# Performance work log

Hardware: AMD Instinct MI355X
Metric: run time of the kernel (lower is better)

The kernel has to match this reference:

```python
import jax, jax.numpy as jnp
import numpy as np
from jax import lax

DN = ('NCHW', 'OIHW', 'NCHW')

def conv3x3(x, w):
    return lax.conv_general_dilated(x, w, (1, 1), 'SAME', dimension_numbers=DN)

def conv1x1(x, w, b):
    # w: [O, C], x: [B, C, H, W]
    return jnp.einsum('oc,bchw->bohw', w, x) + b[None, :, None, None]

def bn_relu(x, p):
    # p: [2, C] -> (scale, shift), eval-mode folded BatchNorm + ReLU
    return jax.nn.relu(x * p[0][None, :, None, None] + p[1][None, :, None, None])

def pam(y, Wb, bb, Wc, bc, Wd, bd, alpha):
    B, C, H, W = y.shape
    n = H * W
    b_ = conv1x1(y, Wb, bb).reshape(B, -1, n)   # [B, C/8, N]
    c_ = conv1x1(y, Wc, bc).reshape(B, -1, n)   # [B, C/8, N]
    d_ = conv1x1(y, Wd, bd).reshape(B, C, n)    # [B, C, N]
    energy = jnp.einsum('bkn,bkm->bnm', b_, c_)  # [B, N, N]
    attn = jax.nn.softmax(energy, axis=-1)
    feat = jnp.einsum('bcm,bnm->bcn', d_, attn).reshape(B, C, H, W)
    return alpha[0] * feat + y

def cam(y, beta):
    B, C, H, W = y.shape
    xf = y.reshape(B, C, H * W)
    energy = jnp.einsum('bcn,bdn->bcd', xf, xf)  # [B, C, C]
    energy = jnp.max(energy, axis=-1, keepdims=True) - energy
    attn = jax.nn.softmax(energy, axis=-1)
    feat = jnp.einsum('bcd,bdn->bcn', attn, xf).reshape(B, C, H, W)
    return beta[0] * feat + y

def reference(x, Wp1, bnp1, Wc1, bnc1, Wb, bb, Wc, bc, Wd, bd, alpha, beta,
              Wp2, bnp2, Wc2, bnc2, Wout, bout, Wp3, bp3, Wc3, bc3):
    feat_p = bn_relu(conv3x3(x, Wp1), bnp1)
    feat_p = pam(feat_p, Wb, bb, Wc, bc, Wd, bd, alpha)
    feat_p = bn_relu(conv3x3(feat_p, Wp2), bnp2)

    feat_c = bn_relu(conv3x3(x, Wc1), bnc1)
    feat_c = cam(feat_c, beta)
    feat_c = bn_relu(conv3x3(feat_c, Wc2), bnc2)

    fusion = feat_p + feat_c
    out_main = jax.nn.sigmoid(conv1x1(fusion, Wout, bout))
    out_p = jax.nn.sigmoid(conv1x1(feat_p, Wp3, bp3))
    out_c = jax.nn.sigmoid(conv1x1(feat_c, Wc3, bc3))
    return (out_main, out_p, out_c)

def setup_inputs() -> dict:
    key = jax.random.key(0)
    ks = jax.random.split(key, 24)
    Cin, Ci, Ck, NC = 512, 128, 16, 19
    B, H, W = 8, 64, 64
    s = lambda k, shape, scale=0.05: jax.random.normal(k, shape, jnp.float32) * scale
    return {
        'x': jax.random.normal(ks[0], (B, Cin, H, W), jnp.float32),
        'Wp1': s(ks[1], (Ci, Cin, 3, 3)), 'bnp1': jnp.stack([jnp.ones(Ci), jnp.zeros(Ci)]),
        'Wc1': s(ks[2], (Ci, Cin, 3, 3)), 'bnc1': jnp.stack([jnp.ones(Ci), jnp.zeros(Ci)]),
        'Wb': s(ks[3], (Ck, Ci)), 'bb': s(ks[4], (Ck,)),
        'Wc': s(ks[5], (Ck, Ci)), 'bc': s(ks[6], (Ck,)),
        'Wd': s(ks[7], (Ci, Ci)), 'bd': s(ks[8], (Ci,)),
        'alpha': jax.random.normal(ks[9], (1,), jnp.float32) * 0.5,
        'beta': jax.random.normal(ks[10], (1,), jnp.float32) * 0.5,
        'Wp2': s(ks[11], (Ci, Ci, 3, 3)), 'bnp2': jnp.stack([jnp.ones(Ci), jnp.zeros(Ci)]),
        'Wc2': s(ks[12], (Ci, Ci, 3, 3)), 'bnc2': jnp.stack([jnp.ones(Ci), jnp.zeros(Ci)]),
        'Wout': s(ks[13], (NC, Ci)), 'bout': s(ks[14], (NC,)),
        'Wp3': s(ks[15], (NC, Ci)), 'bp3': s(ks[16], (NC,)),
        'Wc3': s(ks[17], (NC, Ci)), 'bc3': s(ks[18], (NC,)),
    }
```

## Files before the change

kernel.cpp:

```cpp
#include <hip/hip_runtime.h>
#include <math.h>


typedef __attribute__((ext_vector_type(8)))  short short8;
typedef __attribute__((ext_vector_type(16))) float f32x16;

__device__ inline unsigned short f2bf(float f) {
    union { float f; unsigned u; } v; v.f = f;
    unsigned r = v.u + 0x7fffu + ((v.u >> 16) & 1u);
    return (unsigned short)(r >> 16);
}
__device__ inline float bf2f(unsigned short h) {
    union { unsigned u; float f; } v; v.u = ((unsigned)h) << 16;
    return v.f;
}

__global__ __launch_bounds__(256) void wpack_kernel(
    const float* __restrict__ W, unsigned short* __restrict__ wp, int Cin, int total)
{
    int idx = blockIdx.x * 256 + threadIdx.x;
    if (idx >= total) return;
    int chunk = idx / 18432;
    int rem   = idx - chunk * 18432;
    int tap   = rem >> 11;
    int rem2  = rem & 2047;
    int co    = rem2 >> 4;
    int ci    = rem2 & 15;
    int cin   = (chunk << 4) + ci;
    wp[idx] = f2bf(W[((size_t)co * Cin + cin) * 9 + tap]);
}

__global__ __launch_bounds__(256) void wpack_split_kernel(
    const float* __restrict__ W, unsigned short* __restrict__ wph,
    unsigned short* __restrict__ wpl, int Cin, int total)
{
    int idx = blockIdx.x * 256 + threadIdx.x;
    if (idx >= total) return;
    int chunk = idx / 18432;
    int rem   = idx - chunk * 18432;
    int tap   = rem >> 11;
    int rem2  = rem & 2047;
    int co    = rem2 >> 4;
    int ci    = rem2 & 15;
    int cin   = (chunk << 4) + ci;
    float w = W[((size_t)co * Cin + cin) * 9 + tap];
    unsigned short hi = f2bf(w);
    wph[idx] = hi;
    wpl[idx] = f2bf(w - bf2f(hi));
}

__global__ __launch_bounds__(256) void conv3x3_mfma(
    const void* __restrict__ xin, int in_is_fp32, int Cin,
    const unsigned short* __restrict__ wpack, const float* __restrict__ bn,
    float* __restrict__ out_f32, unsigned short* __restrict__ out_bf)
{
    const int t   = threadIdx.x;
    const int w   = t >> 6;
    const int wy  = w >> 1;
    const int wx  = w & 1;
    const int ln  = t & 63;
    const int l31 = ln & 31;
    const int g   = ln >> 5;
    const int y0  = blockIdx.x << 1;
    const int co0 = blockIdx.y << 6;
    const int b   = blockIdx.z;

    __shared__ __align__(16) unsigned short Xl[4 * 66 * 16];
    __shared__ __align__(16) unsigned short Wl[9 * 64 * 16];

    const f32x16 zero = {0,0,0,0,0,0,0,0,0,0,0,0,0,0,0,0};
    f32x16 acc0 = zero, acc1 = zero;

    const int nchunks = Cin >> 4;
    for (int ch = 0; ch < nchunks; ++ch) {
        const int cin0 = ch << 4;
        for (int pid = t; pid < 264; pid += 256) {
            int r  = pid / 66;
            int xc = pid - r * 66;
            int gy = y0 - 1 + r;
            int gx = xc - 1;
            unsigned short tmp[16];
            if ((unsigned)gy < 64u && (unsigned)gx < 64u) {
                if (in_is_fp32) {
                    const float* src = (const float*)xin
                        + (((size_t)b * Cin + cin0) << 12) + (gy << 6) + gx;
#pragma unroll
                    for (int c = 0; c < 16; c++) tmp[c] = f2bf(src[(size_t)c << 12]);
                } else {
                    const unsigned short* src = (const unsigned short*)xin
                        + (((size_t)b * Cin + cin0) << 12) + (gy << 6) + gx;
#pragma unroll
                    for (int c = 0; c < 16; c++) tmp[c] = src[(size_t)c << 12];
                }
            } else {
#pragma unroll
                for (int c = 0; c < 16; c++) tmp[c] = 0;
            }
            *(uint4*)&Xl[pid * 16 + 0] = ((uint4*)tmp)[0];
            *(uint4*)&Xl[pid * 16 + 8] = ((uint4*)tmp)[1];
        }
        {
            const uint4* wsrc = (const uint4*)wpack;
            const int base = ch * 2304 + (co0 << 1);
            for (int idx = t; idx < 1152; idx += 256)
                ((uint4*)Wl)[idx] = wsrc[base + ((idx >> 7) << 8) + (idx & 127)];
        }
        __syncthreads();

#pragma unroll 3
        for (int tap = 0; tap < 9; ++tap) {
            const int dy = tap / 3, dx = tap - dy * 3;
            short8 a = *(const short8*)&Wl[((tap << 6) + (wy << 5) + l31) * 16 + (g << 3)];
            const int row = wx + dy;
            short8 b0 = *(const short8*)&Xl[(row * 66 + l31 + dx) * 16 + (g << 3)];
            short8 b1 = *(const short8*)&Xl[(row * 66 + l31 + 32 + dx) * 16 + (g << 3)];
            acc0 = __builtin_amdgcn_mfma_f32_32x32x16_bf16(a, b0, acc0, 0, 0, 0);
            acc1 = __builtin_amdgcn_mfma_f32_32x32x16_bf16(a, b1, acc1, 0, 0, 0);
        }
        __syncthreads();
    }

    const int y = y0 + wx;
#pragma unroll
    for (int j = 0; j < 2; j++) {
        const f32x16 a = j ? acc1 : acc0;
#pragma unroll
        for (int r = 0; r < 16; r++) {
            int co = co0 + (wy << 5) + (r & 3) + ((r >> 2) << 3) + (g << 2);
            int x  = (j << 5) + l31;
            float v = fmaf(a[r], bn[co], bn[128 + co]);
            v = v > 0.f ? v : 0.f;
            size_t o = (((size_t)b * 128 + co) << 12) + (y << 6) + x;
            if (out_f32) out_f32[o] = v;
            if (out_bf)  out_bf[o]  = f2bf(v);
        }
    }
}

__global__ __launch_bounds__(256) void conv3x3_mfma_hilo(
    const float* __restrict__ xin, int Cin,
    const unsigned short* __restrict__ wph, const unsigned short* __restrict__ wpl,
    const float* __restrict__ bn, float* __restrict__ out_f32,
    unsigned short* __restrict__ outh, unsigned short* __restrict__ outl)
{
    const int t   = threadIdx.x;
    const int w   = t >> 6;
    const int wy  = w >> 1;
    const int wx  = w & 1;
    const int ln  = t & 63;
    const int l31 = ln & 31;
    const int g   = ln >> 5;
    const int y0  = blockIdx.x << 1;
    const int co0 = blockIdx.y << 6;
    const int b   = blockIdx.z;

    __shared__ __align__(16) unsigned short Xh[4 * 66 * 16];
    __shared__ __align__(16) unsigned short Xo[4 * 66 * 16];
    __shared__ __align__(16) unsigned short Wh[9 * 64 * 16];
    __shared__ __align__(16) unsigned short Wo[9 * 64 * 16];

    const f32x16 zero = {0,0,0,0,0,0,0,0,0,0,0,0,0,0,0,0};
    f32x16 acc0 = zero, acc1 = zero;

    const int nchunks = Cin >> 4;
    for (int ch = 0; ch < nchunks; ++ch) {
        const int cin0 = ch << 4;
        for (int pid = t; pid < 264; pid += 256) {
            int r  = pid / 66;
            int xc = pid - r * 66;
            int gy = y0 - 1 + r;
            int gx = xc - 1;
            unsigned short th[16], tl[16];
            if ((unsigned)gy < 64u && (unsigned)gx < 64u) {
                const float* src = xin + (((size_t)b * Cin + cin0) << 12) + (gy << 6) + gx;
#pragma unroll
                for (int c = 0; c < 16; c++) {
                    float f = src[(size_t)c << 12];
                    unsigned short hi = f2bf(f);
                    th[c] = hi;
                    tl[c] = f2bf(f - bf2f(hi));
                }
            } else {
#pragma unroll
                for (int c = 0; c < 16; c++) { th[c] = 0; tl[c] = 0; }
            }
            *(uint4*)&Xh[pid * 16 + 0] = ((uint4*)th)[0];
            *(uint4*)&Xh[pid * 16 + 8] = ((uint4*)th)[1];
            *(uint4*)&Xo[pid * 16 + 0] = ((uint4*)tl)[0];
            *(uint4*)&Xo[pid * 16 + 8] = ((uint4*)tl)[1];
        }
        {
            const uint4* sh = (const uint4*)wph;
            const uint4* sl = (const uint4*)wpl;
            const int base = ch * 2304 + (co0 << 1);
            for (int idx = t; idx < 1152; idx += 256) {
                int o = base + ((idx >> 7) << 8) + (idx & 127);
                ((uint4*)Wh)[idx] = sh[o];
                ((uint4*)Wo)[idx] = sl[o];
            }
        }
        __syncthreads();

#pragma unroll 1
        for (int tap = 0; tap < 9; ++tap) {
            const int dy = tap / 3, dx = tap - dy * 3;
            const int wi = ((tap << 6) + (wy << 5) + l31) * 16 + (g << 3);
            const int row = wx + dy;
            const int xi0 = (row * 66 + l31 + dx) * 16 + (g << 3);
            const int xi1 = (row * 66 + l31 + 32 + dx) * 16 + (g << 3);
            short8 ah = *(const short8*)&Wh[wi];
            short8 al = *(const short8*)&Wo[wi];
            short8 b0h = *(const short8*)&Xh[xi0];
            short8 b1h = *(const short8*)&Xh[xi1];
            short8 b0l = *(const short8*)&Xo[xi0];
            short8 b1l = *(const short8*)&Xo[xi1];
            acc0 = __builtin_amdgcn_mfma_f32_32x32x16_bf16(ah, b0h, acc0, 0, 0, 0);
            acc1 = __builtin_amdgcn_mfma_f32_32x32x16_bf16(ah, b1h, acc1, 0, 0, 0);
            acc0 = __builtin_amdgcn_mfma_f32_32x32x16_bf16(ah, b0l, acc0, 0, 0, 0);
            acc1 = __builtin_amdgcn_mfma_f32_32x32x16_bf16(ah, b1l, acc1, 0, 0, 0);
            acc0 = __builtin_amdgcn_mfma_f32_32x32x16_bf16(al, b0h, acc0, 0, 0, 0);
            acc1 = __builtin_amdgcn_mfma_f32_32x32x16_bf16(al, b1h, acc1, 0, 0, 0);
        }
        __syncthreads();
    }

    const int y = y0 + wx;
#pragma unroll
    for (int j = 0; j < 2; j++) {
        const f32x16 a = j ? acc1 : acc0;
#pragma unroll
        for (int r = 0; r < 16; r++) {
            int co = co0 + (wy << 5) + (r & 3) + ((r >> 2) << 3) + (g << 2);
            int x  = (j << 5) + l31;
            float v = fmaf(a[r], bn[co], bn[128 + co]);
            v = v > 0.f ? v : 0.f;
            size_t o = (((size_t)b * 128 + co) << 12) + (y << 6) + x;
            out_f32[o] = v;
            if (outh) {
                unsigned short hi = f2bf(v);
                outh[o] = hi;
                outl[o] = f2bf(v - bf2f(hi));
            }
        }
    }
}

__global__ __launch_bounds__(256) void cam_energy_mfma(
    const unsigned short* __restrict__ bh, const unsigned short* __restrict__ bl,
    float* __restrict__ egy_part)
{
    const int t   = threadIdx.x;
    const int w   = t >> 6;
    const int ln  = t & 63;
    const int l31 = ln & 31;
    const int g   = ln >> 5;
    const int i0  = (blockIdx.x >> 2) << 5;
    const int j0  = (blockIdx.x & 3) << 5;
    const int nseg = blockIdx.y;
    const int b   = blockIdx.z;

    __shared__ float red[4][64][17];

    const f32x16 zero = {0,0,0,0,0,0,0,0,0,0,0,0,0,0,0,0};
    f32x16 acc = zero;
    const int nb = (nseg << 9) + (w << 7) + (g << 3);
    const size_t ri = ((size_t)b * 128 + i0 + l31) << 12;
    const size_t rj = ((size_t)b * 128 + j0 + l31) << 12;

#pragma unroll
    for (int c = 0; c < 8; c++) {
        const int n0 = nb + (c << 4);
        short8 ah  = *(const short8*)(bh + ri + n0);
        short8 al  = *(const short8*)(bl + ri + n0);
        short8 bhf = *(const short8*)(bh + rj + n0);
        short8 blf = *(const short8*)(bl + rj + n0);
        acc = __builtin_amdgcn_mfma_f32_32x32x16_bf16(ah, bhf, acc, 0, 0, 0);
        acc = __builtin_amdgcn_mfma_f32_32x32x16_bf16(ah, blf, acc, 0, 0, 0);
        acc = __builtin_amdgcn_mfma_f32_32x32x16_bf16(al, bhf, acc, 0, 0, 0);
    }
#pragma unroll
    for (int r = 0; r < 16; r++) red[w][ln][r] = acc[r];
    __syncthreads();

    const int lane = t & 63;
    const int rq   = t >> 6;
    float* base = egy_part + (((size_t)(nseg * 8 + b)) << 14);
#pragma unroll
    for (int e = 0; e < 4; e++) {
        const int reg = (rq << 2) + e;
        float v = red[0][lane][reg] + red[1][lane][reg]
                + red[2][lane][reg] + red[3][lane][reg];
        const int i = i0 + (reg & 3) + ((reg >> 2) << 3) + ((lane >> 5) << 2);
        base[i * 128 + j0 + (lane & 31)] = v;
    }
}

__global__ __launch_bounds__(256) void cam_softmax_fused(
    const float* __restrict__ egy_part, float* __restrict__ egy)
{
    const int b   = blockIdx.x;
    const int rg  = blockIdx.y;
    const int t   = threadIdx.x;
    const int row = (rg << 4) + (t >> 4);
    const int jg  = t & 15;

    float e[8];
#pragma unroll
    for (int jj = 0; jj < 8; jj++) e[jj] = 0.f;
    for (int seg = 0; seg < 8; seg++) {
        const float* p = egy_part + (((size_t)(seg * 8 + b)) << 14) + row * 128 + (jg << 3);
#pragma unroll
        for (int jj = 0; jj < 8; jj++) e[jj] += p[jj];
    }
    float mn = e[0];
#pragma unroll
    for (int jj = 1; jj < 8; jj++) mn = fminf(mn, e[jj]);
#pragma unroll
    for (int k = 1; k < 16; k <<= 1) mn = fminf(mn, __shfl_xor(mn, k));
    float s = 0.f;
#pragma unroll
    for (int jj = 0; jj < 8; jj++) { float p = __expf(mn - e[jj]); e[jj] = p; s += p; }
#pragma unroll
    for (int k = 1; k < 16; k <<= 1) s += __shfl_xor(s, k);
    const float inv = 1.f / s;
    float* orow = egy + ((size_t)b << 14) + row * 128 + (jg << 3);
#pragma unroll
    for (int jj = 0; jj < 8; jj++) orow[jj] = e[jj] * inv;
}

__global__ __launch_bounds__(256) void pam_qk_1x1(
    const float* __restrict__ A, const float* __restrict__ Wb, const float* __restrict__ bb,
    const float* __restrict__ Wc, const float* __restrict__ bc,
    unsigned short* __restrict__ qt, unsigned short* __restrict__ kt)
{
    __shared__ float wl[2 * 16 * 128];
    __shared__ float bl[32];
    const int t = threadIdx.x;
    const int n = (blockIdx.x << 8) + t;
    const int b = blockIdx.y;
    for (int idx = t; idx < 2048; idx += 256) { wl[idx] = Wb[idx]; wl[2048 + idx] = Wc[idx]; }
    if (t < 16) { bl[t] = bb[t]; bl[16 + t] = bc[t]; }
    __syncthreads();
    float ab[16], ac[16];
#pragma unroll
    for (int k = 0; k < 16; k++) { ab[k] = 0.f; ac[k] = 0.f; }
    for (int chn = 0; chn < 128; ++chn) {
        float a = A[(((size_t)b * 128 + chn) << 12) + n];
#pragma unroll
        for (int k = 0; k < 16; k++) {
            ab[k] = fmaf(wl[k * 128 + chn], a, ab[k]);
            ac[k] = fmaf(wl[2048 + k * 128 + chn], a, ac[k]);
        }
    }
    unsigned short uq[16], uk[16];
#pragma unroll
    for (int k = 0; k < 16; k++) {
        uq[k] = f2bf(ab[k] + bl[k]);
        uk[k] = f2bf(ac[k] + bl[16 + k]);
    }
    size_t row = (size_t)b * 4096 + n;
    ((uint4*)qt)[row * 2 + 0] = ((uint4*)uq)[0];
    ((uint4*)qt)[row * 2 + 1] = ((uint4*)uq)[1];
    ((uint4*)kt)[row * 2 + 0] = ((uint4*)uk)[0];
    ((uint4*)kt)[row * 2 + 1] = ((uint4*)uk)[1];
}

__global__ __launch_bounds__(256) void pam_v_1x1(
    const float* __restrict__ A, const float* __restrict__ Wd, const float* __restrict__ bd,
    unsigned short* __restrict__ vb)
{
    __shared__ float wl[32 * 128];
    __shared__ float bl[32];
    const int t   = threadIdx.x;
    const int n   = (blockIdx.x << 8) + t;
    const int co0 = blockIdx.y << 5;
    const int b   = blockIdx.z;
    for (int idx = t; idx < 4096; idx += 256) {
        int c2 = idx >> 7, chv = idx & 127;
        wl[idx] = Wd[(co0 + c2) * 128 + chv];
    }
    if (t < 32) bl[t] = bd[co0 + t];
    __syncthreads();
    float acc[32];
#pragma unroll
    for (int k = 0; k < 32; k++) acc[k] = 0.f;
    for (int chn = 0; chn < 128; ++chn) {
        float a = A[(((size_t)b * 128 + chn) << 12) + n];
#pragma unroll
        for (int k = 0; k < 32; k++) acc[k] = fmaf(wl[k * 128 + chn], a, acc[k]);
    }
#pragma unroll
    for (int k = 0; k < 32; k++)
        vb[(((size_t)b * 128 + co0 + k) << 12) + n] = f2bf(acc[k] + bl[k]);
}

__global__ __launch_bounds__(256) void pam_rowmax(
    const unsigned short* __restrict__ qt, const unsigned short* __restrict__ kt,
    float* __restrict__ rowmax)
{
    const int t  = threadIdx.x;
    const int w  = t >> 6;
    const int L  = t & 63;
    const int ln = L & 31;
    const int g  = L >> 5;
    const int b  = blockIdx.y;
    const int n0 = blockIdx.x << 5;
    __shared__ float red[4][32];

    const f32x16 zero = {0,0,0,0,0,0,0,0,0,0,0,0,0,0,0,0};
    short8 qfrag = *(const short8*)(qt + (((size_t)b * 4096 + n0 + ln) << 4) + (g << 3));

    float mx = -INFINITY;
    for (int mq = (w << 5); mq < 4096; mq += 128) {
        short8 kfrag = *(const short8*)(kt + (((size_t)b * 4096 + mq + ln) << 4) + (g << 3));
        f32x16 s = __builtin_amdgcn_mfma_f32_32x32x16_bf16(kfrag, qfrag, zero, 0, 0, 0);
#pragma unroll
        for (int r = 0; r < 16; r++) mx = fmaxf(mx, s[r]);
    }
    mx = fmaxf(mx, __shfl_xor(mx, 32));
    if (L < 32) red[w][L] = mx;
    __syncthreads();
    if (t < 32) {
        float m = fmaxf(fmaxf(red[0][t], red[1][t]), fmaxf(red[2][t], red[3][t]));
        rowmax[((size_t)b << 12) + n0 + t] = m;
    }
}

__global__ __launch_bounds__(256) void pam_attn_mfma(
    const unsigned short* __restrict__ qt, const unsigned short* __restrict__ kt,
    const unsigned short* __restrict__ vb, const float* __restrict__ rowmax,
    const float* __restrict__ alpha, const float* __restrict__ Y,
    unsigned short* __restrict__ outb)
{
    const int t  = threadIdx.x;
    const int w  = t >> 6;
    const int L  = t & 63;
    const int ln = L & 31;
    const int g  = L >> 5;
    const int b  = blockIdx.y;
    const int n0 = blockIdx.x << 5;
    const int c0 = w << 5;

    __shared__ unsigned short Pf[16 * 256];
    __shared__ float red[4][32];

    const f32x16 zero = {0,0,0,0,0,0,0,0,0,0,0,0,0,0,0,0};
    short8 qfrag = *(const short8*)(qt + (((size_t)b * 4096 + n0 + ln) << 4) + (g << 3));
    const float rm = rowmax[((size_t)b << 12) + n0 + ln];
    const float al = alpha[0];

    f32x16 acc = zero;
    float rs = 0.f;

    for (int m0 = 0; m0 < 4096; m0 += 128) {
        const int mq = m0 + (w << 5);
        short8 kfrag = *(const short8*)(kt + (((size_t)b * 4096 + mq + ln) << 4) + (g << 3));
        f32x16 s = __builtin_amdgcn_mfma_f32_32x32x16_bf16(kfrag, qfrag, zero, 0, 0, 0);

        float p[16];
#pragma unroll
        for (int r = 0; r < 16; r++) { p[r] = __expf(s[r] - rm); rs += p[r]; }
        float xx[16];
#pragma unroll
        for (int r = 0; r < 16; r++) xx[r] = __shfl_xor(p[r], 32);

        unsigned short f0[8], f1[8];
#pragma unroll
        for (int i = 0; i < 4; i++) {
            f0[i]     = f2bf(g ? xx[4 + i]  : p[i]);
            f0[4 + i] = f2bf(g ? p[4 + i]   : xx[i]);
            f1[i]     = f2bf(g ? xx[12 + i] : p[8 + i]);
            f1[4 + i] = f2bf(g ? p[12 + i]  : xx[8 + i]);
        }
        *(short8*)(&Pf[((w << 2) + g) * 256 + (ln << 3)])     = *(short8*)f0;
        *(short8*)(&Pf[((w << 2) + 2 + g) * 256 + (ln << 3)]) = *(short8*)f1;
        __syncthreads();

#pragma unroll
        for (int kk = 0; kk < 8; kk++) {
            short8 pfrag = *(const short8*)(&Pf[((kk << 1) + g) * 256 + (ln << 3)]);
            short8 vfrag = *(const short8*)(vb + (((size_t)b * 128 + c0 + ln) << 12)
                                               + m0 + (kk << 4) + (g << 3));
            acc = __builtin_amdgcn_mfma_f32_32x32x16_bf16(vfrag, pfrag, acc, 0, 0, 0);
        }
        __syncthreads();
    }

    rs += __shfl_xor(rs, 32);
    if (L < 32) red[w][L] = rs;
    __syncthreads();
    const float inv = 1.f / (red[0][ln] + red[1][ln] + red[2][ln] + red[3][ln]);
    const int n = n0 + ln;
#pragma unroll
    for (int r = 0; r < 16; r++) {
        int c = c0 + (r & 3) + ((r >> 2) << 3) + (g << 2);
        size_t idx = (((size_t)b * 128 + c) << 12) + n;
        outb[idx] = f2bf(fmaf(al, acc[r] * inv, Y[idx]));
    }
}

__global__ __launch_bounds__(256) void cam_feat(
    const float* __restrict__ attn, const float* __restrict__ Bf,
    const float* __restrict__ beta, float* __restrict__ outf)
{
    const int t  = threadIdx.x;
    const int n  = (blockIdx.x << 8) + t;
    const int c0 = blockIdx.y << 5;
    const int b  = blockIdx.z;
    __shared__ float al[32 * 128];
    for (int idx = t; idx < 4096; idx += 256)
        al[idx] = attn[(size_t)b * 16384 + (c0 + (idx >> 7)) * 128 + (idx & 127)];
    __syncthreads();
    float acc[32];
#pragma unroll
    for (int k = 0; k < 32; k++) acc[k] = 0.f;
    for (int d = 0; d < 128; ++d) {
        float v = Bf[(((size_t)b * 128 + d) << 12) + n];
#pragma unroll
        for (int k = 0; k < 32; k++) acc[k] = fmaf(al[k * 128 + d], v, acc[k]);
    }
    float be = beta[0];
#pragma unroll
    for (int k = 0; k < 32; k++) {
        size_t idx = (((size_t)b * 128 + c0 + k) << 12) + n;
        outf[idx] = fmaf(be, acc[k], Bf[idx]);
    }
}

__global__ __launch_bounds__(256) void heads(
    const float* __restrict__ FP, const float* __restrict__ FC,
    const float* __restrict__ Wout, const float* __restrict__ bout,
    const float* __restrict__ Wp3, const float* __restrict__ bp3,
    const float* __restrict__ Wc3, const float* __restrict__ bc3,
    float* __restrict__ out)
{
    const int t = threadIdx.x;
    const int n = (blockIdx.x << 8) + t;
    const int b = blockIdx.y;
    __shared__ float wl[3 * 19 * 128];
    __shared__ float bl[3 * 19];
    for (int idx = t; idx < 2432; idx += 256) {
        wl[idx]        = Wout[idx];
        wl[2432 + idx] = Wp3[idx];
        wl[4864 + idx] = Wc3[idx];
    }
    if (t < 19) { bl[t] = bout[t]; bl[19 + t] = bp3[t]; bl[38 + t] = bc3[t]; }
    __syncthreads();
    float am[19], ap[19], ac[19];
#pragma unroll
    for (int o = 0; o < 19; o++) { am[o] = 0.f; ap[o] = 0.f; ac[o] = 0.f; }
    for (int chn = 0; chn < 128; ++chn) {
        float pv = FP[(((size_t)b * 128 + chn) << 12) + n];
        float cv = FC[(((size_t)b * 128 + chn) << 12) + n];
        float fv = pv + cv;
#pragma unroll
        for (int o = 0; o < 19; o++) {
            am[o] = fmaf(wl[o * 128 + chn], fv, am[o]);
            ap[o] = fmaf(wl[2432 + o * 128 + chn], pv, ap[o]);
            ac[o] = fmaf(wl[4864 + o * 128 + chn], cv, ac[o]);
        }
    }
    const size_t OS = (size_t)8 * 19 * 4096;
#pragma unroll
    for (int o = 0; o < 19; o++) {
        size_t base = (((size_t)b * 19 + o) << 12) + n;
        out[base]          = 1.f / (1.f + __expf(-(am[o] + bl[o])));
        out[OS + base]     = 1.f / (1.f + __expf(-(ap[o] + bl[19 + o])));
        out[2 * OS + base] = 1.f / (1.f + __expf(-(ac[o] + bl[38 + o])));
    }
}

extern "C" void kernel_launch(void* const* d_in, const int* in_sizes, int n_in,
                              void* d_out, int out_size, void* d_ws, size_t ws_size,
                              hipStream_t stream)
{
    const float* x     = (const float*)d_in[0];
    const float* Wp1   = (const float*)d_in[1];
    const float* bnp1  = (const float*)d_in[2];
    const float* Wc1   = (const float*)d_in[3];
    const float* bnc1  = (const float*)d_in[4];
    const float* Wb    = (const float*)d_in[5];
    const float* bb    = (const float*)d_in[6];
    const float* Wc    = (const float*)d_in[7];
    const float* bcv   = (const float*)d_in[8];
    const float* Wd    = (const float*)d_in[9];
    const float* bd    = (const float*)d_in[10];
    const float* alpha = (const float*)d_in[11];
    const float* beta  = (const float*)d_in[12];
    const float* Wp2   = (const float*)d_in[13];
    const float* bnp2  = (const float*)d_in[14];
    const float* Wc2   = (const float*)d_in[15];
    const float* bnc2  = (const float*)d_in[16];
    const float* Wout  = (const float*)d_in[17];
    const float* bo    = (const float*)d_in[18];
    const float* Wp3   = (const float*)d_in[19];
    const float* bp3   = (const float*)d_in[20];
    const float* Wc3   = (const float*)d_in[21];
    const float* bc3   = (const float*)d_in[22];
    float* out = (float*)d_out;

    char* ws = (char*)d_ws;
    const size_t MB = 1u << 20;
    const size_t W1SZ = (size_t)32 * 18432 * 2;
    const size_t W2SZ = (size_t)8 * 18432 * 2;
    float*          bufA     = (float*)(ws);
    float*          bufB     = (float*)(ws + 16 * MB);
    unsigned short* vb       = (unsigned short*)(ws + 32 * MB);
    float*          egy_part = (float*)(ws + 40 * MB);
    float*          bufD     = (float*)(ws + 32 * MB);
    unsigned short* bh       = (unsigned short*)(ws + 48 * MB);
    unsigned short* blo      = (unsigned short*)(ws + 56 * MB);
    unsigned short* pam_bf   = (unsigned short*)(ws + 48 * MB);
    float*          camf     = (float*)(ws + 48 * MB);
    unsigned short* qt       = (unsigned short*)(ws + 64 * MB);
    unsigned short* kt       = (unsigned short*)(ws + 65 * MB);
    float*          rowmax   = (float*)(ws + 66 * MB);
    float*          egy      = (float*)(ws + 66 * MB + (1u << 17));
    unsigned short* wp1      = (unsigned short*)(ws + 67 * MB);
    unsigned short* wc1h     = (unsigned short*)(ws + 67 * MB + W1SZ);
    unsigned short* wc1l     = (unsigned short*)(ws + 67 * MB + 2 * W1SZ);
    unsigned short* wp2      = (unsigned short*)(ws + 67 * MB + 3 * W1SZ);
    unsigned short* wc2h     = (unsigned short*)(ws + 67 * MB + 3 * W1SZ + W2SZ);
    unsigned short* wc2l     = (unsigned short*)(ws + 67 * MB + 3 * W1SZ + 2 * W2SZ);

    dim3 blk(256);
    const int n1 = 32 * 18432;
    const int n2 = 8 * 18432;
    wpack_kernel<<<dim3((n1 + 255) / 256), blk, 0, stream>>>(Wp1, wp1, 512, n1);
    wpack_kernel<<<dim3((n2 + 255) / 256), blk, 0, stream>>>(Wp2, wp2, 128, n2);
    wpack_split_kernel<<<dim3((n1 + 255) / 256), blk, 0, stream>>>(Wc1, wc1h, wc1l, 512, n1);
    wpack_split_kernel<<<dim3((n2 + 255) / 256), blk, 0, stream>>>(Wc2, wc2h, wc2l, 128, n2);

    conv3x3_mfma<<<dim3(32, 2, 8), blk, 0, stream>>>(x, 1, 512, wp1, bnp1, bufA, (unsigned short*)0);
    conv3x3_mfma_hilo<<<dim3(32, 2, 8), blk, 0, stream>>>(x, 512, wc1h, wc1l, bnc1, bufB, bh, blo);
    cam_energy_mfma<<<dim3(16, 8, 8), blk, 0, stream>>>(bh, blo, egy_part);
    cam_softmax_fused<<<dim3(8, 8), blk, 0, stream>>>(egy_part, egy);
    pam_qk_1x1<<<dim3(16, 8), blk, 0, stream>>>(bufA, Wb, bb, Wc, bcv, qt, kt);
    pam_v_1x1<<<dim3(16, 4, 8), blk, 0, stream>>>(bufA, Wd, bd, vb);
    pam_rowmax<<<dim3(128, 8), blk, 0, stream>>>(qt, kt, rowmax);
    pam_attn_mfma<<<dim3(128, 8), blk, 0, stream>>>(qt, kt, vb, rowmax, alpha, bufA, pam_bf);
    conv3x3_mfma<<<dim3(32, 2, 8), blk, 0, stream>>>(pam_bf, 0, 128, wp2, bnp2, bufD, (unsigned short*)0);
    cam_feat<<<dim3(16, 4, 8), blk, 0, stream>>>(egy, bufB, beta, camf);
    conv3x3_mfma_hilo<<<dim3(32, 2, 8), blk, 0, stream>>>(camf, 128, wc2h, wc2l, bnc2, bufA,
                                                          (unsigned short*)0, (unsigned short*)0);
    heads<<<dim3(16, 8), blk, 0, stream>>>(bufD, bufA, Wout, bo, Wp3, bp3, Wc3, bc3, out);
}
```

Baseline: 841.6 us.

## Pre-split inputs into channel-blocked bf16 hi/lo layout for conv staging

Adds a kernel that converts the fp32 input once into bf16 hi/lo tensors laid out as [B][C/16][H*W][16]. The 3x3 conv kernels then stage tiles with contiguous 16-byte vector loads instead of strided per-channel scalar loads and per-chunk float-to-bf16 conversion. The PAM output and the CAM feature kernel now write this blocked layout directly. The CAM path drops its fp32 intermediate and reconstructs values from hi/lo. This removes redundant uncoalesced gathers and conversions repeated across output-channel blocks, at the cost of an extra pass and more workspace memory.

```diff
diff --git a/kernel.cpp b/kernel.cpp
--- a/kernel.cpp
+++ b/kernel.cpp
@@ -49,10 +49,35 @@
     wpl[idx] = f2bf(w - bf2f(hi));
 }
 
+__global__ __launch_bounds__(256) void x_split_kernel(
+    const float* __restrict__ x, unsigned short* __restrict__ xh,
+    unsigned short* __restrict__ xl)
+{
+    const int ch = blockIdx.x;
+    const int b  = blockIdx.y;
+    const int t  = threadIdx.x;
+    for (int seg = 0; seg < 16; ++seg) {
+        const int n = (seg << 8) + t;
+        unsigned short uh[16], ul[16];
+#pragma unroll
+        for (int c = 0; c < 16; ++c) {
+            float f = x[(((size_t)b * 512 + (ch << 4) + c) << 12) + n];
+            unsigned short hi = f2bf(f);
+            uh[c] = hi;
+            ul[c] = f2bf(f - bf2f(hi));
+        }
+        size_t dst = ((((size_t)b * 32 + ch) << 12) + n) << 4;
+        *(uint4*)(xh + dst)     = ((uint4*)uh)[0];
+        *(uint4*)(xh + dst + 8) = ((uint4*)uh)[1];
+        *(uint4*)(xl + dst)     = ((uint4*)ul)[0];
+        *(uint4*)(xl + dst + 8) = ((uint4*)ul)[1];
+    }
+}
+
 __global__ __launch_bounds__(256) void conv3x3_mfma(
-    const void* __restrict__ xin, int in_is_fp32, int Cin,
+    const unsigned short* __restrict__ xb, int Cin,
     const unsigned short* __restrict__ wpack, const float* __restrict__ bn,
-    float* __restrict__ out_f32, unsigned short* __restrict__ out_bf)
+    float* __restrict__ out_f32)
 {
     const int t   = threadIdx.x;
     const int w   = t >> 6;
@@ -64,40 +89,31 @@
     const int y0  = blockIdx.x << 1;
     const int co0 = blockIdx.y << 6;
     const int b   = blockIdx.z;
+    const int nc16 = Cin >> 4;
 
     __shared__ __align__(16) unsigned short Xl[4 * 66 * 16];
     __shared__ __align__(16) unsigned short Wl[9 * 64 * 16];
 
+    if (t < 8) {
+        int r = t >> 1, xc = (t & 1) * 65;
+        uint4 z = {0, 0, 0, 0};
+        *(uint4*)&Xl[(r * 66 + xc) * 16 + 0] = z;
+        *(uint4*)&Xl[(r * 66 + xc) * 16 + 8] = z;
+    }
+
     const f32x16 zero = {0,0,0,0,0,0,0,0,0,0,0,0,0,0,0,0};
     f32x16 acc0 = zero, acc1 = zero;
 
-    const int nchunks = Cin >> 4;
-    for (int ch = 0; ch < nchunks; ++ch) {
-        const int cin0 = ch << 4;
-        for (int pid = t; pid < 264; pid += 256) {
-            int r  = pid / 66;
-            int xc = pid - r * 66;
+    for (int ch = 0; ch < nc16; ++ch) {
+#pragma unroll
+        for (int it = 0; it < 2; ++it) {
+            int idx = t + (it << 8);
+            int r = idx >> 7, u = idx & 127;
             int gy = y0 - 1 + r;
-            int gx = xc - 1;
-            unsigned short tmp[16];
-            if ((unsigned)gy < 64u && (unsigned)gx < 64u) {
-                if (in_is_fp32) {
-                    const float* src = (const float*)xin
-                        + (((size_t)b * Cin + cin0) << 12) + (gy << 6) + gx;
-#pragma unroll
-                    for (int c = 0; c < 16; c++) tmp[c] = f2bf(src[(size_t)c << 12]);
-                } else {
-                    const unsigned short* src = (const unsigned short*)xin
-                        + (((size_t)b * Cin + cin0) << 12) + (gy << 6) + gx;
-#pragma unroll
-                    for (int c = 0; c < 16; c++) tmp[c] = src[(size_t)c << 12];
-                }
-            } else {
-#pragma unroll
-                for (int c = 0; c < 16; c++) tmp[c] = 0;
-            }
-            *(uint4*)&Xl[pid * 16 + 0] = ((uint4*)tmp)[0];
-            *(uint4*)&Xl[pid * 16 + 8] = ((uint4*)tmp)[1];
+            uint4 val = {0, 0, 0, 0};
+            if ((unsigned)gy < 64u)
+                val = *(const uint4*)(xb + ((((size_t)(b * nc16 + ch)) << 12) + (gy << 6)) * 16 + (u << 3));
+            *(uint4*)&Xl[(r * 66 + 1) * 16 + (u << 3)] = val;
         }
         {
             const uint4* wsrc = (const uint4*)wpack;
@@ -130,16 +146,14 @@
             int x  = (j << 5) + l31;
             float v = fmaf(a[r], bn[co], bn[128 + co]);
             v = v > 0.f ? v : 0.f;
-            size_t o = (((size_t)b * 128 + co) << 12) + (y << 6) + x;
-            if (out_f32) out_f32[o] = v;
-            if (out_bf)  out_bf[o]  = f2bf(v);
+            out_f32[(((size_t)b * 128 + co) << 12) + (y << 6) + x] = v;
         }
     }
 }
 
 __global__ __launch_bounds__(256) void conv3x3_mfma_hilo(
-    const float* __restrict__ xin, int Cin,
-    const unsigned short* __restrict__ wph, const unsigned short* __restrict__ wpl,
+    const unsigned short* __restrict__ xbh, const unsigned short* __restrict__ xbl,
+    int Cin, const unsigned short* __restrict__ wph, const unsigned short* __restrict__ wpl,
     const float* __restrict__ bn, float* __restrict__ out_f32,
     unsigned short* __restrict__ outh, unsigned short* __restrict__ outl)
 {
@@ -153,41 +167,39 @@
     const int y0  = blockIdx.x << 1;
     const int co0 = blockIdx.y << 6;
     const int b   = blockIdx.z;
+    const int nc16 = Cin >> 4;
 
     __shared__ __align__(16) unsigned short Xh[4 * 66 * 16];
     __shared__ __align__(16) unsigned short Xo[4 * 66 * 16];
     __shared__ __align__(16) unsigned short Wh[9 * 64 * 16];
     __shared__ __align__(16) unsigned short Wo[9 * 64 * 16];
 
+    if (t < 8) {
+        int r = t >> 1, xc = (t & 1) * 65;
+        uint4 z = {0, 0, 0, 0};
+        *(uint4*)&Xh[(r * 66 + xc) * 16 + 0] = z;
+        *(uint4*)&Xh[(r * 66 + xc) * 16 + 8] = z;
+        *(uint4*)&Xo[(r * 66 + xc) * 16 + 0] = z;
+        *(uint4*)&Xo[(r * 66 + xc) * 16 + 8] = z;
+    }
+
     const f32x16 zero = {0,0,0,0,0,0,0,0,0,0,0,0,0,0,0,0};
     f32x16 acc0 = zero, acc1 = zero;
 
-    const int nchunks = Cin >> 4;
-    for (int ch = 0; ch < nchunks; ++ch) {
-        const int cin0 = ch << 4;
-        for (int pid = t; pid < 264; pid += 256) {
-            int r  = pid / 66;
-            int xc = pid - r * 66;
+    for (int ch = 0; ch < nc16; ++ch) {
+#pragma unroll
+        for (int it = 0; it < 2; ++it) {
+            int idx = t + (it << 8);
+            int r = idx >> 7, u = idx & 127;
             int gy = y0 - 1 + r;
-            int gx = xc - 1;
-            unsigned short th[16], tl[16];
-            if ((unsigned)gy < 64u && (unsigned)gx < 64u) {
-                const float* src = xin + (((size_t)b * Cin + cin0) << 12) + (gy << 6) + gx;
-#pragma unroll
-                for (int c = 0; c < 16; c++) {
-                    float f = src[(size_t)c << 12];
-                    unsigned short hi = f2bf(f);
-                    th[c] = hi;
-                    tl[c] = f2bf(f - bf2f(hi));
-                }
-            } else {
-#pragma unroll
-                for (int c = 0; c < 16; c++) { th[c] = 0; tl[c] = 0; }
+            uint4 vh = {0, 0, 0, 0}, vl = {0, 0, 0, 0};
+            if ((unsigned)gy < 64u) {
+                size_t o = ((((size_t)(b * nc16 + ch)) << 12) + (gy << 6)) * 16 + (u << 3);
+                vh = *(const uint4*)(xbh + o);
+                vl = *(const uint4*)(xbl + o);
             }
-            *(uint4*)&Xh[pid * 16 + 0] = ((uint4*)th)[0];
-            *(uint4*)&Xh[pid * 16 + 8] = ((uint4*)th)[1];
-            *(uint4*)&Xo[pid * 16 + 0] = ((uint4*)tl)[0];
-            *(uint4*)&Xo[pid * 16 + 8] = ((uint4*)tl)[1];
+            *(uint4*)&Xh[(r * 66 + 1) * 16 + (u << 3)] = vh;
+            *(uint4*)&Xo[(r * 66 + 1) * 16 + (u << 3)] = vl;
         }
         {
             const uint4* sh = (const uint4*)wph;
@@ -235,7 +247,7 @@
             float v = fmaf(a[r], bn[co], bn[128 + co]);
             v = v > 0.f ? v : 0.f;
             size_t o = (((size_t)b * 128 + co) << 12) + (y << 6) + x;
-            out_f32[o] = v;
+            if (out_f32) out_f32[o] = v;
             if (outh) {
                 unsigned short hi = f2bf(v);
                 outh[o] = hi;
@@ -494,14 +506,16 @@
 #pragma unroll
     for (int r = 0; r < 16; r++) {
         int c = c0 + (r & 3) + ((r >> 2) << 3) + (g << 2);
-        size_t idx = (((size_t)b * 128 + c) << 12) + n;
-        outb[idx] = f2bf(fmaf(al, acc[r] * inv, Y[idx]));
+        size_t yi = (((size_t)b * 128 + c) << 12) + n;
+        size_t oo = ((((size_t)b * 8 + (c >> 4)) << 12) + n) * 16 + (c & 15);
+        outb[oo] = f2bf(fmaf(al, acc[r] * inv, Y[yi]));
     }
 }
 
 __global__ __launch_bounds__(256) void cam_feat(
-    const float* __restrict__ attn, const float* __restrict__ Bf,
-    const float* __restrict__ beta, float* __restrict__ outf)
+    const float* __restrict__ attn, const unsigned short* __restrict__ bh,
+    const unsigned short* __restrict__ blo, const float* __restrict__ beta,
+    unsigned short* __restrict__ camh, unsigned short* __restrict__ caml)
 {
     const int t  = threadIdx.x;
     const int n  = (blockIdx.x << 8) + t;
@@ -509,22 +523,39 @@
     const int b  = blockIdx.z;
     __shared__ float al[32 * 128];
     for (int idx = t; idx < 4096; idx += 256)
-        al[idx] = attn[(size_t)b * 16384 + (c0 + (idx >> 7)) * 128 + (idx & 127)];
+        al[idx] = attn[((size_t)b << 14) + (c0 + (idx >> 7)) * 128 + (idx & 127)];
     __syncthreads();
     float acc[32];
 #pragma unroll
     for (int k = 0; k < 32; k++) acc[k] = 0.f;
     for (int d = 0; d < 128; ++d) {
-        float v = Bf[(((size_t)b * 128 + d) << 12) + n];
+        size_t idx = (((size_t)b * 128 + d) << 12) + n;
+        float v = bf2f(bh[idx]) + bf2f(blo[idx]);
 #pragma unroll
         for (int k = 0; k < 32; k++) acc[k] = fmaf(al[k * 128 + d], v, acc[k]);
     }
     float be = beta[0];
+    unsigned short oh[32], ol[32];
 #pragma unroll
     for (int k = 0; k < 32; k++) {
         size_t idx = (((size_t)b * 128 + c0 + k) << 12) + n;
-        outf[idx] = fmaf(be, acc[k], Bf[idx]);
-    }
+        float bfv = bf2f(bh[idx]) + bf2f(blo[idx]);
+        float v = fmaf(be, acc[k], bfv);
+        unsigned short hi = f2bf(v);
+        oh[k] = hi;
+        ol[k] = f2bf(v - bf2f(hi));
+    }
+    const int g0 = c0 >> 4;
+    size_t d0 = ((((size_t)b * 8 + g0) << 12) + n) << 4;
+    size_t d1 = ((((size_t)b * 8 + g0 + 1) << 12) + n) << 4;
+    *(uint4*)(camh + d0)     = ((uint4*)oh)[0];
+    *(uint4*)(camh + d0 + 8) = ((uint4*)oh)[1];
+    *(uint4*)(camh + d1)     = ((uint4*)oh)[2];
+    *(uint4*)(camh + d1 + 8) = ((uint4*)oh)[3];
+    *(uint4*)(caml + d0)     = ((uint4*)ol)[0];
+    *(uint4*)(caml + d0 + 8) = ((uint4*)ol)[1];
+    *(uint4*)(caml + d1)     = ((uint4*)ol)[2];
+    *(uint4*)(caml + d1 + 8) = ((uint4*)ol)[3];
 }
 
 __global__ __launch_bounds__(256) void heads(
@@ -604,24 +635,26 @@
     const size_t W1SZ = (size_t)32 * 18432 * 2;
     const size_t W2SZ = (size_t)8 * 18432 * 2;
     float*          bufA     = (float*)(ws);
-    float*          bufB     = (float*)(ws + 16 * MB);
-    unsigned short* vb       = (unsigned short*)(ws + 32 * MB);
-    float*          egy_part = (float*)(ws + 40 * MB);
-    float*          bufD     = (float*)(ws + 32 * MB);
-    unsigned short* bh       = (unsigned short*)(ws + 48 * MB);
-    unsigned short* blo      = (unsigned short*)(ws + 56 * MB);
-    unsigned short* pam_bf   = (unsigned short*)(ws + 48 * MB);
-    float*          camf     = (float*)(ws + 48 * MB);
-    unsigned short* qt       = (unsigned short*)(ws + 64 * MB);
-    unsigned short* kt       = (unsigned short*)(ws + 65 * MB);
-    float*          rowmax   = (float*)(ws + 66 * MB);
-    float*          egy      = (float*)(ws + 66 * MB + (1u << 17));
-    unsigned short* wp1      = (unsigned short*)(ws + 67 * MB);
-    unsigned short* wc1h     = (unsigned short*)(ws + 67 * MB + W1SZ);
-    unsigned short* wc1l     = (unsigned short*)(ws + 67 * MB + 2 * W1SZ);
-    unsigned short* wp2      = (unsigned short*)(ws + 67 * MB + 3 * W1SZ);
-    unsigned short* wc2h     = (unsigned short*)(ws + 67 * MB + 3 * W1SZ + W2SZ);
-    unsigned short* wc2l     = (unsigned short*)(ws + 67 * MB + 3 * W1SZ + 2 * W2SZ);
+    unsigned short* bh       = (unsigned short*)(ws + 16 * MB);
+    unsigned short* blo      = (unsigned short*)(ws + 24 * MB);
+    unsigned short* xh       = (unsigned short*)(ws + 32 * MB);
+    unsigned short* xl       = (unsigned short*)(ws + 64 * MB);
+    float*          egy_part = (float*)(ws + 32 * MB);
+    unsigned short* qt       = (unsigned short*)(ws + 36 * MB);
+    unsigned short* kt       = (unsigned short*)(ws + 37 * MB);
+    float*          rowmax   = (float*)(ws + 38 * MB);
+    float*          egy      = (float*)(ws + 38 * MB + (1u << 18));
+    unsigned short* vb       = (unsigned short*)(ws + 40 * MB);
+    float*          bufD     = (float*)(ws + 48 * MB);
+    unsigned short* pam_bfB  = (unsigned short*)(ws + 64 * MB);
+    unsigned short* camh     = (unsigned short*)(ws + 72 * MB);
+    unsigned short* caml     = (unsigned short*)(ws + 80 * MB);
+    unsigned short* wp1      = (unsigned short*)(ws + 96 * MB);
+    unsigned short* wc1h     = (unsigned short*)(ws + 96 * MB + W1SZ);
+    unsigned short* wc1l     = (unsigned short*)(ws + 96 * MB + 2 * W1SZ);
+    unsigned short* wp2      = (unsigned short*)(ws + 96 * MB + 3 * W1SZ);
+    unsigned short* wc2h     = (unsigned short*)(ws + 96 * MB + 3 * W1SZ + W2SZ);
+    unsigned short* wc2l     = (unsigned short*)(ws + 96 * MB + 3 * W1SZ + 2 * W2SZ);
 
     dim3 blk(256);
     const int n1 = 32 * 18432;
@@ -631,17 +664,20 @@
     wpack_split_kernel<<<dim3((n1 + 255) / 256), blk, 0, stream>>>(Wc1, wc1h, wc1l, 512, n1);
     wpack_split_kernel<<<dim3((n2 + 255) / 256), blk, 0, stream>>>(Wc2, wc2h, wc2l, 128, n2);
 
-    conv3x3_mfma<<<dim3(32, 2, 8), blk, 0, stream>>>(x, 1, 512, wp1, bnp1, bufA, (unsigned short*)0);
-    conv3x3_mfma_hilo<<<dim3(32, 2, 8), blk, 0, stream>>>(x, 512, wc1h, wc1l, bnc1, bufB, bh, blo);
+    x_split_kernel<<<dim3(32, 8), blk, 0, stream>>>(x, xh, xl);
+
+    conv3x3_mfma<<<dim3(32, 2, 8), blk, 0, stream>>>(xh, 512, wp1, bnp1, bufA);
+    conv3x3_mfma_hilo<<<dim3(32, 2, 8), blk, 0, stream>>>(xh, xl, 512, wc1h, wc1l, bnc1,
+                                                          (float*)0, bh, blo);
     cam_energy_mfma<<<dim3(16, 8, 8), blk, 0, stream>>>(bh, blo, egy_part);
     cam_softmax_fused<<<dim3(8, 8), blk, 0, stream>>>(egy_part, egy);
     pam_qk_1x1<<<dim3(16, 8), blk, 0, stream>>>(bufA, Wb, bb, Wc, bcv, qt, kt);
     pam_v_1x1<<<dim3(16, 4, 8), blk, 0, stream>>>(bufA, Wd, bd, vb);
     pam_rowmax<<<dim3(128, 8), blk, 0, stream>>>(qt, kt, rowmax);
-    pam_attn_mfma<<<dim3(128, 8), blk, 0, stream>>>(qt, kt, vb, rowmax, alpha, bufA, pam_bf);
-    conv3x3_mfma<<<dim3(32, 2, 8), blk, 0, stream>>>(pam_bf, 0, 128, wp2, bnp2, bufD, (unsigned short*)0);
-    cam_feat<<<dim3(16, 4, 8), blk, 0, stream>>>(egy, bufB, beta, camf);
-    conv3x3_mfma_hilo<<<dim3(32, 2, 8), blk, 0, stream>>>(camf, 128, wc2h, wc2l, bnc2, bufA,
-                                                          (unsigned short*)0, (unsigned short*)0);
+    pam_attn_mfma<<<dim3(128, 8), blk, 0, stream>>>(qt, kt, vb, rowmax, alpha, bufA, pam_bfB);
+    conv3x3_mfma<<<dim3(32, 2, 8), blk, 0, stream>>>(pam_bfB, 128, wp2, bnp2, bufD);
+    cam_feat<<<dim3(16, 4, 8), blk, 0, stream>>>(egy, bh, blo, beta, camh, caml);
+    conv3x3_mfma_hilo<<<dim3(32, 2, 8), blk, 0, stream>>>(camh, caml, 128, wc2h, wc2l, bnc2,
+                                                          bufA, (unsigned short*)0, (unsigned short*)0);
     heads<<<dim3(16, 8), blk, 0, stream>>>(bufD, bufA, Wout, bo, Wp3, bp3, Wc3, bc3, out);
 }
```

After: 893.4 us. 6.2% more time.
